# Kernel optimization log

Measured on AMD Instinct MI355X. Metric: run time of the kernel, lower is better.

## Reference

```python
import jax, jax.numpy as jnp
import numpy as np

COS_EPS = 1e-8   # torch F.cosine_similarity norm clamp
SIM_EPS = 1e-6   # +1e-6 added to every cosine similarity in get_cossim
LOG_EPS = 1e-6   # +1e-6 inside log in calc_loss


def setup_inputs() -> dict:
    key = jax.random.key(0)
    k1, = jax.random.split(key, 1)
    N, M, D = 1024, 16, 512
    embeddings = jax.random.normal(k1, (N, M, D), dtype=jnp.float32)
    w = jnp.asarray(10.0, dtype=jnp.float32)
    b = jnp.asarray(-5.0, dtype=jnp.float32)
    return {"embeddings": embeddings, "w": w, "b": b}


def _unit(x):
    n = jnp.sqrt(jnp.sum(x * x, axis=-1, keepdims=True))
    return x / jnp.maximum(n, COS_EPS)


def _ge2e_loss(embeddings, w, b):
    N, M, D = embeddings.shape
    e_unit = _unit(embeddings)                              # [N, M, D]

    # full centroids (mean over utterances)
    centroids = jnp.mean(embeddings, axis=1)                # [N, D]
    c_unit = _unit(centroids)                               # [N, D]

    # cosine sim of every utterance vs every speaker centroid
    cossim = jnp.einsum('nmd,kd->nmk', e_unit, c_unit)      # [N, M, N]

    # leave-one-out centroid for own-speaker entries (self-exclusion)
    loo = (jnp.sum(embeddings, axis=1, keepdims=True) - embeddings) / (M - 1)  # [N, M, D]
    diag = jnp.sum(e_unit * _unit(loo), axis=-1)            # [N, M]

    idx = jnp.arange(N)
    cossim = cossim.at[idx, :, idx].set(diag)
    cossim = cossim + SIM_EPS

    sim_matrix = w * cossim + b                             # [N, M, N]

    pos = sim_matrix[idx, :, idx]                           # [N, M]
    neg = jnp.log(jnp.sum(jnp.exp(sim_matrix), axis=2) + LOG_EPS)  # [N, M]
    return jnp.sum(neg - pos)


def reference(embeddings, w, b):
    return _ge2e_loss(embeddings, w, b)
```

## Files before the change

kernel.cpp:

```cpp
#include <hip/hip_runtime.h>

#define N_SPK 1024
#define M_UTT 16
#define D_DIM 512

typedef __attribute__((ext_vector_type(8))) short bf16x8;
typedef __attribute__((ext_vector_type(4))) float f32x4;

__device__ __forceinline__ float wave_sum64(float v) {
  #pragma unroll
  for (int off = 32; off >= 1; off >>= 1) v += __shfl_xor(v, off, 64);
  return v;
}

__device__ __forceinline__ unsigned short f2bf(float x) {
  unsigned int u = __float_as_uint(x);
  unsigned int r = (u + 0x7FFFu + ((u >> 16) & 1u)) >> 16;
  return (unsigned short)r;
}

__device__ __forceinline__ unsigned int pack_bf16(float a, float b) {
  return (unsigned int)f2bf(a) | ((unsigned int)f2bf(b) << 16);
}

__device__ __forceinline__ void gload_lds16(const void* g, void* l) {
  __builtin_amdgcn_global_load_lds(
      (const __attribute__((address_space(1))) void*)g,
      (__attribute__((address_space(3))) void*)l, 16, 0, 0);
}

__global__ __launch_bounds__(256) void prep_kernel(
    const float* __restrict__ emb, const float* __restrict__ wp,
    const float* __restrict__ bp, unsigned int* __restrict__ eU,
    unsigned int* __restrict__ cU, float* __restrict__ pos_out)
{
  const int n = blockIdx.x;
  const int t = threadIdx.x;
  __shared__ float es[M_UTT * D_DIM];
  __shared__ float Sd[D_DIM];
  __shared__ float red[4];
  __shared__ float inv_s[M_UTT];

  const float* base = emb + (size_t)n * (M_UTT * D_DIM);
  #pragma unroll
  for (int i = 0; i < 8; ++i) {
    int s = t + i * 256;
    reinterpret_cast<float4*>(es)[s] = reinterpret_cast<const float4*>(base)[s];
  }
  __syncthreads();

  #pragma unroll
  for (int rep = 0; rep < 2; ++rep) {
    int d = t + rep * 256;
    float s = 0.f;
    #pragma unroll
    for (int m = 0; m < M_UTT; ++m) s += es[m * D_DIM + d];
    Sd[d] = s;
  }
  __syncthreads();

  float p = 0.f;
  #pragma unroll
  for (int rep = 0; rep < 2; ++rep) {
    int d = t + rep * 256;
    float c = Sd[d] * (1.f / M_UTT);
    p += c * c;
  }
  p = wave_sum64(p);
  if ((t & 63) == 0) red[t >> 6] = p;
  __syncthreads();
  float cn2 = red[0] + red[1] + red[2] + red[3];
  float invc = 1.f / fmaxf(sqrtf(cn2), 1e-8f);

  {
    int d = t * 2;
    float c0 = Sd[d] * (1.f / M_UTT) * invc;
    float c1 = Sd[d + 1] * (1.f / M_UTT) * invc;
    cU[n * 256 + t] = pack_bf16(c0, c1);
  }

  const int wid = t >> 6, lane = t & 63;
  const float w = *wp, b = *bp;
  for (int m = wid; m < M_UTT; m += 4) {
    float dot = 0.f, ne = 0.f, nl = 0.f;
    #pragma unroll
    for (int r = 0; r < 8; ++r) {
      int d = lane + r * 64;
      float e = es[m * D_DIM + d];
      float l = Sd[d] - e;
      dot += e * l; ne += e * e; nl += l * l;
    }
    dot = wave_sum64(dot); ne = wave_sum64(ne); nl = wave_sum64(nl);
    if (lane == 0) {
      float inv_e = 1.f / fmaxf(sqrtf(ne), 1e-8f);
      float inv_l = 1.f / fmaxf(sqrtf(nl) * (1.f / (M_UTT - 1)), 1e-8f);
      float diag = dot * (1.f / (M_UTT - 1)) * inv_e * inv_l;
      pos_out[n * M_UTT + m] = w * (diag + 1e-6f) + b;
      inv_s[m] = inv_e;
    }
  }
  __syncthreads();

  #pragma unroll
  for (int i = 0; i < 16; ++i) {
    int p2 = t + i * 256;
    int m = p2 >> 8;
    int d = (p2 & 255) * 2;
    float sc = inv_s[m];
    float x0 = es[m * D_DIM + d] * sc;
    float x1 = es[m * D_DIM + d + 1] * sc;
    eU[(size_t)n * 4096 + p2] = pack_bf16(x0, x1);
  }
}

#define NTILES 16

struct StageOff { unsigned int gA0, gA1, gB0, gB1; int c0off, c1off; };

__device__ __forceinline__ void stage_tile(
    const char* __restrict__ eU, const char* __restrict__ cU,
    char* AsB, int t, const StageOff& so)
{
  const int buf = t & 3;
  const int d0b = t * 64;
  char* Ab = AsB + buf * 16384;
  char* Bb = AsB + 65536 + buf * 16384;
  gload_lds16(eU + so.gA0 + d0b, Ab + so.c0off);
  gload_lds16(eU + so.gA1 + d0b, Ab + so.c1off);
  gload_lds16(cU + so.gB0 + d0b, Bb + so.c0off);
  gload_lds16(cU + so.gB1 + d0b, Bb + so.c1off);
}

__device__ __forceinline__ void compute_tile(
    const char* AsB, int t, int wm, int wn, int laneoff, f32x4 acc[8][4])
{
  const int buf = t & 3;
  const char* Ab = AsB + buf * 16384;
  const char* Bb = AsB + 65536 + buf * 16384;
  bf16x8 af[8], bfr[4];
  #pragma unroll
  for (int mi = 0; mi < 8; ++mi)
    af[mi] = *reinterpret_cast<const bf16x8*>(Ab + (wm * 128 + mi * 16) * 64 + laneoff);
  #pragma unroll
  for (int nj = 0; nj < 4; ++nj)
    bfr[nj] = *reinterpret_cast<const bf16x8*>(Bb + (wn * 64 + nj * 16) * 64 + laneoff);
  __builtin_amdgcn_s_setprio(1);
  #pragma unroll
  for (int mi = 0; mi < 8; ++mi)
    #pragma unroll
    for (int nj = 0; nj < 4; ++nj)
      acc[mi][nj] = __builtin_amdgcn_mfma_f32_16x16x32_bf16(
          af[mi], bfr[nj], acc[mi][nj], 0, 0, 0);
  __builtin_amdgcn_s_setprio(0);
}

__global__ __launch_bounds__(512, 2) void mfma_kernel(
    const char* __restrict__ eU, const char* __restrict__ cU,
    const float* __restrict__ pos, const float* __restrict__ wp,
    const float* __restrict__ bp, float* __restrict__ partial)
{
  __shared__ char AsB[131072];
  __shared__ float pos_l[256];
  __shared__ float rowsum[4][256];

  const int t = threadIdx.x;
  const int lane = t & 63;
  const int wv = t >> 6;
  const int wm = wv >> 2, wn = wv & 3;

  const int bid = blockIdx.x;
  const int sw = (bid & 7) * 32 + (bid >> 3);
  const int cb = sw & 3, rb = sw >> 2;
  const int row0 = rb * 256, col0 = cb * 256;

  const float w = *wp, b = *bp;
  const float bb = w * 1e-6f + b;

  if (t < 256) pos_l[t] = pos[row0 + t];

  StageOff so;
  {
    const int seg = (lane & 7) ^ (lane >> 3);
    const int p = seg >> 2, ks = seg & 3;
    const int rA0 = ((2 * wv) * 8 + (lane >> 3)) * 2 + p;
    const int rA1 = ((2 * wv + 1) * 8 + (lane >> 3)) * 2 + p;
    so.gA0 = (unsigned int)(row0 + rA0) * 1024u + ks * 16;
    so.gA1 = (unsigned int)(row0 + rA1) * 1024u + ks * 16;
    so.gB0 = (unsigned int)(col0 + rA0) * 1024u + ks * 16;
    so.gB1 = (unsigned int)(col0 + rA1) * 1024u + ks * 16;
    so.c0off = (2 * wv) * 1024;
    so.c1off = (2 * wv + 1) * 1024;
  }
  const int j = lane & 15, g = lane >> 4;
  const int laneoff = (j >> 1) * 128 + ((((j & 1) * 4 + g) ^ (j >> 1)) * 16);

  f32x4 acc[8][4] = {};

  __syncthreads();

  stage_tile(eU, cU, AsB, 0, so);
  stage_tile(eU, cU, AsB, 1, so);
  stage_tile(eU, cU, AsB, 2, so);

  for (int tt = 0; tt < NTILES - 2; ++tt) {
    asm volatile("s_waitcnt vmcnt(8)" ::: "memory");
    __builtin_amdgcn_s_barrier();
    if (tt < NTILES - 3) stage_tile(eU, cU, AsB, tt + 3, so);
    compute_tile(AsB, tt, wm, wn, laneoff, acc);
    __builtin_amdgcn_s_barrier();
  }
  asm volatile("s_waitcnt vmcnt(4)" ::: "memory");
  __builtin_amdgcn_s_barrier();
  compute_tile(AsB, NTILES - 2, wm, wn, laneoff, acc);
  __builtin_amdgcn_s_barrier();
  asm volatile("s_waitcnt vmcnt(0)" ::: "memory");
  __builtin_amdgcn_s_barrier();
  compute_tile(AsB, NTILES - 1, wm, wn, laneoff, acc);

  float esum[8][4];
  #pragma unroll
  for (int mi = 0; mi < 8; ++mi)
    #pragma unroll
    for (int rg = 0; rg < 4; ++rg) esum[mi][rg] = 0.f;

  #pragma unroll
  for (int nj = 0; nj < 4; ++nj) {
    const int kg = col0 + wn * 64 + nj * 16 + (lane & 15);
    #pragma unroll
    for (int mi = 0; mi < 8; ++mi) {
      #pragma unroll
      for (int rg = 0; rg < 4; ++rg) {
        const int r_loc = wm * 128 + mi * 16 + (lane >> 4) * 4 + rg;
        float arg = w * acc[mi][nj][rg] + bb;
        if (kg == ((row0 + r_loc) >> 4)) arg = pos_l[r_loc];
        esum[mi][rg] += __expf(arg);
      }
    }
  }
  #pragma unroll
  for (int mi = 0; mi < 8; ++mi)
    #pragma unroll
    for (int rg = 0; rg < 4; ++rg) {
      float v = esum[mi][rg];
      v += __shfl_xor(v, 1, 64);
      v += __shfl_xor(v, 2, 64);
      v += __shfl_xor(v, 4, 64);
      v += __shfl_xor(v, 8, 64);
      esum[mi][rg] = v;
    }
  if ((lane & 15) == 0) {
    #pragma unroll
    for (int mi = 0; mi < 8; ++mi)
      #pragma unroll
      for (int rg = 0; rg < 4; ++rg)
        rowsum[wn][wm * 128 + mi * 16 + (lane >> 4) * 4 + rg] = esum[mi][rg];
  }
  __syncthreads();
  if (t < 256)
    partial[(size_t)cb * (N_SPK * M_UTT) + row0 + t] =
        rowsum[0][t] + rowsum[1][t] + rowsum[2][t] + rowsum[3][t];
}

__global__ __launch_bounds__(256) void finalize_kernel(
    const float* __restrict__ partial, const float* __restrict__ pos,
    float* __restrict__ bsum)
{
  const int t = threadIdx.x;
  const int r = blockIdx.x * 256 + t;
  float s = 0.f;
  #pragma unroll
  for (int cb = 0; cb < 4; ++cb) s += partial[cb * (N_SPK * M_UTT) + r];
  float v = logf(s + 1e-6f) - pos[r];
  v = wave_sum64(v);
  __shared__ float red[4];
  if ((t & 63) == 0) red[t >> 6] = v;
  __syncthreads();
  if (t == 0) bsum[blockIdx.x] = red[0] + red[1] + red[2] + red[3];
}

__global__ void final_reduce(const float* __restrict__ bsum,
                             float* __restrict__ out)
{
  float v = bsum[threadIdx.x];
  v = wave_sum64(v);
  if (threadIdx.x == 0) out[0] = v;
}

extern "C" void kernel_launch(void* const* d_in, const int* in_sizes, int n_in,
                              void* d_out, int out_size, void* d_ws, size_t ws_size,
                              hipStream_t stream) {
  const float* emb = (const float*)d_in[0];
  const float* wp  = (const float*)d_in[1];
  const float* bp  = (const float*)d_in[2];
  float* out = (float*)d_out;

  char* wsb = (char*)d_ws;
  unsigned int* eU  = (unsigned int*)wsb;
  unsigned int* cU  = (unsigned int*)(wsb + 16777216);
  float* pos        = (float*)(wsb + 16777216 + 1048576);
  float* partial    = (float*)(wsb + 16777216 + 1048576 + 65536);
  float* bsum       = (float*)(wsb + 16777216 + 1048576 + 65536 + 262144);

  prep_kernel<<<N_SPK, 256, 0, stream>>>(emb, wp, bp, eU, cU, pos);
  mfma_kernel<<<256, 512, 0, stream>>>(
      (const char*)eU, (const char*)cU, pos, wp, bp, partial);
  finalize_kernel<<<(N_SPK * M_UTT) / 256, 256, 0, stream>>>(partial, pos, bsum);
  final_reduce<<<1, 64, 0, stream>>>(bsum, out);
}
```

Baseline: 45.67 us.

## Shrink MFMA tile to 128x256 with 4 waves, triple buffering, fuse final reduction

The GEMM block tile changes from 256x256 with 8 waves to 128x256 with 4 waves, and the grid grows from 256 to 512 blocks so more blocks share the CUs. The LDS pipeline drops from four buffers with three tiles in flight to three buffers with prefetch distance two, which cuts shared memory per block. The finalize and final_reduce kernels merge into one 1024-thread single-block kernel, removing a launch. In exchange, each block reuses fewer B loads per A row, and the single-block reduction serializes the final step.

```diff
diff --git a/kernel.cpp b/kernel.cpp
--- a/kernel.cpp
+++ b/kernel.cpp
@@ -114,36 +114,40 @@
 }
 
 #define NTILES 16
-
-struct StageOff { unsigned int gA0, gA1, gB0, gB1; int c0off, c1off; };
+#define BUFSZ 24576
+
+struct StageOff {
+  unsigned int gA0, gA1, gB0, gB1, gB2, gB3;
+  int a0, a1, b0, b1, b2, b3;
+};
 
 __device__ __forceinline__ void stage_tile(
     const char* __restrict__ eU, const char* __restrict__ cU,
-    char* AsB, int t, const StageOff& so)
-{
-  const int buf = t & 3;
-  const int d0b = t * 64;
-  char* Ab = AsB + buf * 16384;
-  char* Bb = AsB + 65536 + buf * 16384;
-  gload_lds16(eU + so.gA0 + d0b, Ab + so.c0off);
-  gload_lds16(eU + so.gA1 + d0b, Ab + so.c1off);
-  gload_lds16(cU + so.gB0 + d0b, Bb + so.c0off);
-  gload_lds16(cU + so.gB1 + d0b, Bb + so.c1off);
+    char* AsB, int tt, const StageOff& so)
+{
+  char* buf = AsB + (tt % 3) * BUFSZ;
+  const int d0 = tt * 64;
+  gload_lds16(eU + so.gA0 + d0, buf + so.a0);
+  gload_lds16(eU + so.gA1 + d0, buf + so.a1);
+  gload_lds16(cU + so.gB0 + d0, buf + 8192 + so.b0);
+  gload_lds16(cU + so.gB1 + d0, buf + 8192 + so.b1);
+  gload_lds16(cU + so.gB2 + d0, buf + 8192 + so.b2);
+  gload_lds16(cU + so.gB3 + d0, buf + 8192 + so.b3);
 }
 
 __device__ __forceinline__ void compute_tile(
-    const char* AsB, int t, int wm, int wn, int laneoff, f32x4 acc[8][4])
-{
-  const int buf = t & 3;
-  const char* Ab = AsB + buf * 16384;
-  const char* Bb = AsB + 65536 + buf * 16384;
+    const char* AsB, int tt, int wv, int laneoff, f32x4 acc[8][4])
+{
+  const char* Ab = AsB + (tt % 3) * BUFSZ;
+  const char* Bb = Ab + 8192;
   bf16x8 af[8], bfr[4];
   #pragma unroll
   for (int mi = 0; mi < 8; ++mi)
-    af[mi] = *reinterpret_cast<const bf16x8*>(Ab + (wm * 128 + mi * 16) * 64 + laneoff);
+    af[mi] = *reinterpret_cast<const bf16x8*>(Ab + mi * 1024 + laneoff);
   #pragma unroll
   for (int nj = 0; nj < 4; ++nj)
-    bfr[nj] = *reinterpret_cast<const bf16x8*>(Bb + (wn * 64 + nj * 16) * 64 + laneoff);
+    bfr[nj] = *reinterpret_cast<const bf16x8*>(
+        Bb + wv * 4096 + nj * 1024 + laneoff);
   __builtin_amdgcn_s_setprio(1);
   #pragma unroll
   for (int mi = 0; mi < 8; ++mi)
@@ -154,42 +158,47 @@
   __builtin_amdgcn_s_setprio(0);
 }
 
-__global__ __launch_bounds__(512, 2) void mfma_kernel(
+__global__ __launch_bounds__(256, 2) void mfma_kernel(
     const char* __restrict__ eU, const char* __restrict__ cU,
     const float* __restrict__ pos, const float* __restrict__ wp,
     const float* __restrict__ bp, float* __restrict__ partial)
 {
-  __shared__ char AsB[131072];
-  __shared__ float pos_l[256];
-  __shared__ float rowsum[4][256];
+  __shared__ char AsB[3 * BUFSZ];
+  __shared__ float pos_l[128];
+  __shared__ float rowsum[4][128];
 
   const int t = threadIdx.x;
   const int lane = t & 63;
   const int wv = t >> 6;
-  const int wm = wv >> 2, wn = wv & 3;
 
   const int bid = blockIdx.x;
-  const int sw = (bid & 7) * 32 + (bid >> 3);
-  const int cb = sw & 3, rb = sw >> 2;
-  const int row0 = rb * 256, col0 = cb * 256;
+  const int sw = (bid & 7) * 64 + (bid >> 3);
+  const int cb = sw >> 7, rb = sw & 127;
+  const int row0 = rb * 128, col0 = cb * 256;
 
   const float w = *wp, b = *bp;
   const float bb = w * 1e-6f + b;
 
-  if (t < 256) pos_l[t] = pos[row0 + t];
+  if (t < 128) pos_l[t] = pos[row0 + t];
 
   StageOff so;
   {
-    const int seg = (lane & 7) ^ (lane >> 3);
+    const int rp = lane >> 3;
+    const int seg = (lane & 7) ^ rp;
     const int p = seg >> 2, ks = seg & 3;
-    const int rA0 = ((2 * wv) * 8 + (lane >> 3)) * 2 + p;
-    const int rA1 = ((2 * wv + 1) * 8 + (lane >> 3)) * 2 + p;
-    so.gA0 = (unsigned int)(row0 + rA0) * 1024u + ks * 16;
-    so.gA1 = (unsigned int)(row0 + rA1) * 1024u + ks * 16;
-    so.gB0 = (unsigned int)(col0 + rA0) * 1024u + ks * 16;
-    so.gB1 = (unsigned int)(col0 + rA1) * 1024u + ks * 16;
-    so.c0off = (2 * wv) * 1024;
-    so.c1off = (2 * wv + 1) * 1024;
+    const int rloc = 2 * rp + p;
+    so.gA0 = (unsigned int)(row0 + (wv * 2 + 0) * 16 + rloc) * 1024u + ks * 16;
+    so.gA1 = (unsigned int)(row0 + (wv * 2 + 1) * 16 + rloc) * 1024u + ks * 16;
+    so.gB0 = (unsigned int)(col0 + (wv * 4 + 0) * 16 + rloc) * 1024u + ks * 16;
+    so.gB1 = (unsigned int)(col0 + (wv * 4 + 1) * 16 + rloc) * 1024u + ks * 16;
+    so.gB2 = (unsigned int)(col0 + (wv * 4 + 2) * 16 + rloc) * 1024u + ks * 16;
+    so.gB3 = (unsigned int)(col0 + (wv * 4 + 3) * 16 + rloc) * 1024u + ks * 16;
+    so.a0 = (wv * 2 + 0) * 1024;
+    so.a1 = (wv * 2 + 1) * 1024;
+    so.b0 = (wv * 4 + 0) * 1024;
+    so.b1 = (wv * 4 + 1) * 1024;
+    so.b2 = (wv * 4 + 2) * 1024;
+    so.b3 = (wv * 4 + 3) * 1024;
   }
   const int j = lane & 15, g = lane >> 4;
   const int laneoff = (j >> 1) * 128 + ((((j & 1) * 4 + g) ^ (j >> 1)) * 16);
@@ -200,22 +209,17 @@
 
   stage_tile(eU, cU, AsB, 0, so);
   stage_tile(eU, cU, AsB, 1, so);
-  stage_tile(eU, cU, AsB, 2, so);
-
-  for (int tt = 0; tt < NTILES - 2; ++tt) {
-    asm volatile("s_waitcnt vmcnt(8)" ::: "memory");
+
+  for (int tt = 0; tt < NTILES; ++tt) {
+    if (tt < NTILES - 1)
+      asm volatile("s_waitcnt vmcnt(6)" ::: "memory");
+    else
+      asm volatile("s_waitcnt vmcnt(0)" ::: "memory");
     __builtin_amdgcn_s_barrier();
-    if (tt < NTILES - 3) stage_tile(eU, cU, AsB, tt + 3, so);
-    compute_tile(AsB, tt, wm, wn, laneoff, acc);
+    if (tt + 2 < NTILES) stage_tile(eU, cU, AsB, tt + 2, so);
+    compute_tile(AsB, tt, wv, laneoff, acc);
     __builtin_amdgcn_s_barrier();
   }
-  asm volatile("s_waitcnt vmcnt(4)" ::: "memory");
-  __builtin_amdgcn_s_barrier();
-  compute_tile(AsB, NTILES - 2, wm, wn, laneoff, acc);
-  __builtin_amdgcn_s_barrier();
-  asm volatile("s_waitcnt vmcnt(0)" ::: "memory");
-  __builtin_amdgcn_s_barrier();
-  compute_tile(AsB, NTILES - 1, wm, wn, laneoff, acc);
 
   float esum[8][4];
   #pragma unroll
@@ -225,12 +229,12 @@
 
   #pragma unroll
   for (int nj = 0; nj < 4; ++nj) {
-    const int kg = col0 + wn * 64 + nj * 16 + (lane & 15);
+    const int kg = col0 + wv * 64 + nj * 16 + (lane & 15);
     #pragma unroll
     for (int mi = 0; mi < 8; ++mi) {
       #pragma unroll
       for (int rg = 0; rg < 4; ++rg) {
-        const int r_loc = wm * 128 + mi * 16 + (lane >> 4) * 4 + rg;
+        const int r_loc = mi * 16 + (lane >> 4) * 4 + rg;
         float arg = w * acc[mi][nj][rg] + bb;
         if (kg == ((row0 + r_loc) >> 4)) arg = pos_l[r_loc];
         esum[mi][rg] += __expf(arg);
@@ -253,37 +257,37 @@
     for (int mi = 0; mi < 8; ++mi)
       #pragma unroll
       for (int rg = 0; rg < 4; ++rg)
-        rowsum[wn][wm * 128 + mi * 16 + (lane >> 4) * 4 + rg] = esum[mi][rg];
-  }
-  __syncthreads();
-  if (t < 256)
+        rowsum[wv][mi * 16 + (lane >> 4) * 4 + rg] = esum[mi][rg];
+  }
+  __syncthreads();
+  if (t < 128)
     partial[(size_t)cb * (N_SPK * M_UTT) + row0 + t] =
         rowsum[0][t] + rowsum[1][t] + rowsum[2][t] + rowsum[3][t];
 }
 
-__global__ __launch_bounds__(256) void finalize_kernel(
+__global__ __launch_bounds__(1024) void finalize_kernel(
     const float* __restrict__ partial, const float* __restrict__ pos,
-    float* __restrict__ bsum)
+    float* __restrict__ out)
 {
   const int t = threadIdx.x;
-  const int r = blockIdx.x * 256 + t;
-  float s = 0.f;
-  #pragma unroll
-  for (int cb = 0; cb < 4; ++cb) s += partial[cb * (N_SPK * M_UTT) + r];
-  float v = logf(s + 1e-6f) - pos[r];
+  float v = 0.f;
+  #pragma unroll
+  for (int i = 0; i < 16; ++i) {
+    const int r = t + i * 1024;
+    float s = partial[r] + partial[16384 + r] + partial[32768 + r] +
+              partial[49152 + r];
+    v += logf(s + 1e-6f) - pos[r];
+  }
   v = wave_sum64(v);
-  __shared__ float red[4];
+  __shared__ float red[16];
   if ((t & 63) == 0) red[t >> 6] = v;
   __syncthreads();
-  if (t == 0) bsum[blockIdx.x] = red[0] + red[1] + red[2] + red[3];
-}
-
-__global__ void final_reduce(const float* __restrict__ bsum,
-                             float* __restrict__ out)
-{
-  float v = bsum[threadIdx.x];
-  v = wave_sum64(v);
-  if (threadIdx.x == 0) out[0] = v;
+  if (t == 0) {
+    float s = 0.f;
+    #pragma unroll
+    for (int i = 0; i < 16; ++i) s += red[i];
+    out[0] = s;
+  }
 }
 
 extern "C" void kernel_launch(void* const* d_in, const int* in_sizes, int n_in,
@@ -299,11 +303,9 @@
   unsigned int* cU  = (unsigned int*)(wsb + 16777216);
   float* pos        = (float*)(wsb + 16777216 + 1048576);
   float* partial    = (float*)(wsb + 16777216 + 1048576 + 65536);
-  float* bsum       = (float*)(wsb + 16777216 + 1048576 + 65536 + 262144);
 
   prep_kernel<<<N_SPK, 256, 0, stream>>>(emb, wp, bp, eU, cU, pos);
-  mfma_kernel<<<256, 512, 0, stream>>>(
+  mfma_kernel<<<512, 256, 0, stream>>>(
       (const char*)eU, (const char*)cU, pos, wp, bp, partial);
-  finalize_kernel<<<(N_SPK * M_UTT) / 256, 256, 0, stream>>>(partial, pos, bsum);
-  final_reduce<<<1, 64, 0, stream>>>(bsum, out);
-}
+  finalize_kernel<<<1, 1024, 0, stream>>>(partial, pos, out);
+}
```

Measured after the change: 48.62 us. +6.5%, slower.

## Restructure GEMM K-loop into larger double-buffered tiles with interleaved staging

Applied to the files above, without the earlier changes.

The MFMA kernel's K loop now uses 8 tiles of 128 bytes per row, double-buffered in separate A and B LDS arrays, instead of 16 tiles of 64 bytes in a 4-deep ring. Each tile's compute is split into four MFMA quadrants, with LDS fragment reads and async global-to-LDS loads for later tiles interleaved between them and pinned with sched_barrier/s_barrier. The aim is better overlap of memory traffic with matrix math and fewer loop iterations. Separately, the finalize and final_reduce kernels are merged into a single 1024-thread block, removing one launch but serialising the reduction onto one CU.

```diff
diff --git a/kernel.cpp b/kernel.cpp
--- a/kernel.cpp
+++ b/kernel.cpp
@@ -27,6 +27,17 @@
   __builtin_amdgcn_global_load_lds(
       (const __attribute__((address_space(1))) void*)g,
       (__attribute__((address_space(3))) void*)l, 16, 0, 0);
+}
+
+__device__ __forceinline__ void barrier_pin() {
+  __builtin_amdgcn_sched_barrier(0);
+  __builtin_amdgcn_s_barrier();
+  __builtin_amdgcn_sched_barrier(0);
+}
+
+__device__ __forceinline__ void lgkm0() {
+  asm volatile("s_waitcnt lgkmcnt(0)" ::: "memory");
+  __builtin_amdgcn_sched_barrier(0);
 }
 
 __global__ __launch_bounds__(256) void prep_kernel(
@@ -113,44 +124,40 @@
   }
 }
 
-#define NTILES 16
-
-struct StageOff { unsigned int gA0, gA1, gB0, gB1; int c0off, c1off; };
-
-__device__ __forceinline__ void stage_tile(
-    const char* __restrict__ eU, const char* __restrict__ cU,
-    char* AsB, int t, const StageOff& so)
-{
-  const int buf = t & 3;
-  const int d0b = t * 64;
-  char* Ab = AsB + buf * 16384;
-  char* Bb = AsB + 65536 + buf * 16384;
-  gload_lds16(eU + so.gA0 + d0b, Ab + so.c0off);
-  gload_lds16(eU + so.gA1 + d0b, Ab + so.c1off);
-  gload_lds16(cU + so.gB0 + d0b, Bb + so.c0off);
-  gload_lds16(cU + so.gB1 + d0b, Bb + so.c1off);
-}
-
-__device__ __forceinline__ void compute_tile(
-    const char* AsB, int t, int wm, int wn, int laneoff, f32x4 acc[8][4])
-{
-  const int buf = t & 3;
-  const char* Ab = AsB + buf * 16384;
-  const char* Bb = AsB + 65536 + buf * 16384;
-  bf16x8 af[8], bfr[4];
-  #pragma unroll
-  for (int mi = 0; mi < 8; ++mi)
-    af[mi] = *reinterpret_cast<const bf16x8*>(Ab + (wm * 128 + mi * 16) * 64 + laneoff);
-  #pragma unroll
-  for (int nj = 0; nj < 4; ++nj)
-    bfr[nj] = *reinterpret_cast<const bf16x8*>(Bb + (wn * 64 + nj * 16) * 64 + laneoff);
+#define NKT 8
+
+struct Pipe {
+  const char* gA;
+  const char* gB;
+  char* lA;
+  char* lB;
+};
+
+__device__ __forceinline__ void stage_A(const Pipe& p, int tt, int hi) {
+  char* d = p.lA + ((tt & 1) << 15) + hi * 16384;
+  const char* g = p.gA + tt * 128 + hi * 131072;
+  gload_lds16(g, d);
+  gload_lds16(g + 65536, d + 8192);
+}
+__device__ __forceinline__ void stage_B(const Pipe& p, int tt, int hi) {
+  char* d = p.lB + ((tt & 1) << 15) + hi * 16384;
+  const char* g = p.gB + tt * 128 + hi * 131072;
+  gload_lds16(g, d);
+  gload_lds16(g + 65536, d + 8192);
+}
+
+template <int MI0, int NJ0>
+__device__ __forceinline__ void mfma_quad(f32x4 acc[8][4], const bf16x8 af[4][2],
+                                          const bf16x8 bf[4][2]) {
   __builtin_amdgcn_s_setprio(1);
   #pragma unroll
-  for (int mi = 0; mi < 8; ++mi)
-    #pragma unroll
-    for (int nj = 0; nj < 4; ++nj)
-      acc[mi][nj] = __builtin_amdgcn_mfma_f32_16x16x32_bf16(
-          af[mi], bfr[nj], acc[mi][nj], 0, 0, 0);
+  for (int kk = 0; kk < 2; ++kk)
+    #pragma unroll
+    for (int mi = 0; mi < 4; ++mi)
+      #pragma unroll
+      for (int nj = 0; nj < 2; ++nj)
+        acc[MI0 + mi][NJ0 + nj] = __builtin_amdgcn_mfma_f32_16x16x32_bf16(
+            af[mi][kk], bf[NJ0 + nj][kk], acc[MI0 + mi][NJ0 + nj], 0, 0, 0);
   __builtin_amdgcn_s_setprio(0);
 }
 
@@ -159,7 +166,8 @@
     const float* __restrict__ pos, const float* __restrict__ wp,
     const float* __restrict__ bp, float* __restrict__ partial)
 {
-  __shared__ char AsB[131072];
+  __shared__ char ldsA[65536];
+  __shared__ char ldsB[65536];
   __shared__ float pos_l[256];
   __shared__ float rowsum[4][256];
 
@@ -178,44 +186,81 @@
 
   if (t < 256) pos_l[t] = pos[row0 + t];
 
-  StageOff so;
+  Pipe p;
   {
+    const int rowl = wv * 8 + (lane >> 3);
     const int seg = (lane & 7) ^ (lane >> 3);
-    const int p = seg >> 2, ks = seg & 3;
-    const int rA0 = ((2 * wv) * 8 + (lane >> 3)) * 2 + p;
-    const int rA1 = ((2 * wv + 1) * 8 + (lane >> 3)) * 2 + p;
-    so.gA0 = (unsigned int)(row0 + rA0) * 1024u + ks * 16;
-    so.gA1 = (unsigned int)(row0 + rA1) * 1024u + ks * 16;
-    so.gB0 = (unsigned int)(col0 + rA0) * 1024u + ks * 16;
-    so.gB1 = (unsigned int)(col0 + rA1) * 1024u + ks * 16;
-    so.c0off = (2 * wv) * 1024;
-    so.c1off = (2 * wv + 1) * 1024;
-  }
-  const int j = lane & 15, g = lane >> 4;
-  const int laneoff = (j >> 1) * 128 + ((((j & 1) * 4 + g) ^ (j >> 1)) * 16);
+    p.gA = eU + (size_t)(row0 + rowl) * 1024 + seg * 16;
+    p.gB = cU + (size_t)(col0 + rowl) * 1024 + seg * 16;
+    p.lA = ldsA + wv * 1024;
+    p.lB = ldsB + wv * 1024;
+  }
+
+  const int j16 = lane & 15, g = lane >> 4;
+  const int afb0 = (wm * 128 + j16) * 128 + (((0 * 4 + g) ^ (lane & 7)) * 16);
+  const int afb1 = (wm * 128 + j16) * 128 + (((1 * 4 + g) ^ (lane & 7)) * 16);
+  const int bfb0 = (wn * 64 + j16) * 128 + (((0 * 4 + g) ^ (lane & 7)) * 16);
+  const int bfb1 = (wn * 64 + j16) * 128 + (((1 * 4 + g) ^ (lane & 7)) * 16);
 
   f32x4 acc[8][4] = {};
-
-  __syncthreads();
-
-  stage_tile(eU, cU, AsB, 0, so);
-  stage_tile(eU, cU, AsB, 1, so);
-  stage_tile(eU, cU, AsB, 2, so);
-
-  for (int tt = 0; tt < NTILES - 2; ++tt) {
-    asm volatile("s_waitcnt vmcnt(8)" ::: "memory");
-    __builtin_amdgcn_s_barrier();
-    if (tt < NTILES - 3) stage_tile(eU, cU, AsB, tt + 3, so);
-    compute_tile(AsB, tt, wm, wn, laneoff, acc);
-    __builtin_amdgcn_s_barrier();
-  }
+  bf16x8 af[4][2], bf[4][2];
+
+  __syncthreads();
+
+  stage_B(p, 0, 0); stage_B(p, 0, 1);
+  stage_A(p, 0, 0); stage_A(p, 0, 1);
+  stage_B(p, 1, 0); stage_B(p, 1, 1);
   asm volatile("s_waitcnt vmcnt(4)" ::: "memory");
-  __builtin_amdgcn_s_barrier();
-  compute_tile(AsB, NTILES - 2, wm, wn, laneoff, acc);
-  __builtin_amdgcn_s_barrier();
-  asm volatile("s_waitcnt vmcnt(0)" ::: "memory");
-  __builtin_amdgcn_s_barrier();
-  compute_tile(AsB, NTILES - 1, wm, wn, laneoff, acc);
+  __builtin_amdgcn_sched_barrier(0);
+  barrier_pin();
+
+  for (int j = 0; j < NKT; ++j) {
+    const int bo = (j & 1) << 15;
+    #pragma unroll
+    for (int a = 0; a < 4; ++a) {
+      af[a][0] = *reinterpret_cast<const bf16x8*>(ldsA + bo + afb0 + a * 2048);
+      af[a][1] = *reinterpret_cast<const bf16x8*>(ldsA + bo + afb1 + a * 2048);
+    }
+    #pragma unroll
+    for (int nq = 0; nq < 2; ++nq) {
+      bf[nq][0] = *reinterpret_cast<const bf16x8*>(ldsB + bo + bfb0 + nq * 2048);
+      bf[nq][1] = *reinterpret_cast<const bf16x8*>(ldsB + bo + bfb1 + nq * 2048);
+    }
+    if (j <= 6) stage_A(p, j + 1, 0);
+    barrier_pin();
+    lgkm0();
+    mfma_quad<0, 0>(acc, af, bf);
+    barrier_pin();
+    #pragma unroll
+    for (int nq = 2; nq < 4; ++nq) {
+      bf[nq][0] = *reinterpret_cast<const bf16x8*>(ldsB + bo + bfb0 + nq * 2048);
+      bf[nq][1] = *reinterpret_cast<const bf16x8*>(ldsB + bo + bfb1 + nq * 2048);
+    }
+    if (j <= 6) stage_A(p, j + 1, 1);
+    barrier_pin();
+    lgkm0();
+    mfma_quad<0, 2>(acc, af, bf);
+    barrier_pin();
+    #pragma unroll
+    for (int a = 0; a < 4; ++a) {
+      af[a][0] = *reinterpret_cast<const bf16x8*>(ldsA + bo + afb0 + (a + 4) * 2048);
+      af[a][1] = *reinterpret_cast<const bf16x8*>(ldsA + bo + afb1 + (a + 4) * 2048);
+    }
+    if (j <= 5) stage_B(p, j + 2, 0);
+    barrier_pin();
+    lgkm0();
+    mfma_quad<4, 0>(acc, af, bf);
+    barrier_pin();
+    if (j <= 5) stage_B(p, j + 2, 1);
+    if (j < 7) {
+      if (j == 6) { asm volatile("s_waitcnt vmcnt(0)" ::: "memory"); }
+      else        { asm volatile("s_waitcnt vmcnt(4)" ::: "memory"); }
+      __builtin_amdgcn_sched_barrier(0);
+    }
+    barrier_pin();
+    mfma_quad<4, 2>(acc, af, bf);
+    barrier_pin();
+  }
 
   float esum[8][4];
   #pragma unroll
@@ -261,29 +306,29 @@
         rowsum[0][t] + rowsum[1][t] + rowsum[2][t] + rowsum[3][t];
 }
 
-__global__ __launch_bounds__(256) void finalize_kernel(
+__global__ __launch_bounds__(1024) void finalize_kernel(
     const float* __restrict__ partial, const float* __restrict__ pos,
-    float* __restrict__ bsum)
+    float* __restrict__ out)
 {
   const int t = threadIdx.x;
-  const int r = blockIdx.x * 256 + t;
-  float s = 0.f;
-  #pragma unroll
-  for (int cb = 0; cb < 4; ++cb) s += partial[cb * (N_SPK * M_UTT) + r];
-  float v = logf(s + 1e-6f) - pos[r];
+  float v = 0.f;
+  #pragma unroll
+  for (int i = 0; i < 16; ++i) {
+    const int r = t + i * 1024;
+    float s = partial[r] + partial[16384 + r] + partial[32768 + r] +
+              partial[49152 + r];
+    v += logf(s + 1e-6f) - pos[r];
+  }
   v = wave_sum64(v);
-  __shared__ float red[4];
+  __shared__ float red[16];
   if ((t & 63) == 0) red[t >> 6] = v;
   __syncthreads();
-  if (t == 0) bsum[blockIdx.x] = red[0] + red[1] + red[2] + red[3];
-}
-
-__global__ void final_reduce(const float* __restrict__ bsum,
-                             float* __restrict__ out)
-{
-  float v = bsum[threadIdx.x];
-  v = wave_sum64(v);
-  if (threadIdx.x == 0) out[0] = v;
+  if (t == 0) {
+    float s = 0.f;
+    #pragma unroll
+    for (int i = 0; i < 16; ++i) s += red[i];
+    out[0] = s;
+  }
 }
 
 extern "C" void kernel_launch(void* const* d_in, const int* in_sizes, int n_in,
@@ -299,11 +344,9 @@
   unsigned int* cU  = (unsigned int*)(wsb + 16777216);
   float* pos        = (float*)(wsb + 16777216 + 1048576);
   float* partial    = (float*)(wsb + 16777216 + 1048576 + 65536);
-  float* bsum       = (float*)(wsb + 16777216 + 1048576 + 65536 + 262144);
 
   prep_kernel<<<N_SPK, 256, 0, stream>>>(emb, wp, bp, eU, cU, pos);
   mfma_kernel<<<256, 512, 0, stream>>>(
       (const char*)eU, (const char*)cU, pos, wp, bp, partial);
-  finalize_kernel<<<(N_SPK * M_UTT) / 256, 256, 0, stream>>>(partial, pos, bsum);
-  final_reduce<<<1, 64, 0, stream>>>(bsum, out);
-}
+  finalize_kernel<<<1, 1024, 0, stream>>>(partial, pos, out);
+}
```

Measured after the change: 44.87 us. About the same (-1.8%).
